# Optimization experiments

Measured on AMD Instinct MI355X. Metric: run time of the kernel, lower is better.

## Reference

```python
import jax, jax.numpy as jnp
import numpy as np

N_NODES = 50000
N_EDGES = 800000
IN_DIM = 100

def setup_inputs() -> dict:
    key = jax.random.key(0)
    ks = jax.random.split(key, 12)
    nf = jax.random.normal(ks[0], (3, IN_DIM), dtype=jnp.float32)
    tid = jax.random.randint(ks[1], (N_NODES,), 0, 4)
    xr = jax.random.normal(ks[2], (N_NODES, IN_DIM), dtype=jnp.float32)
    # nodes of type 0/1/2 get exact prototype rows; type 3 ('edge') gets random rows
    x = jnp.where((tid < 3)[:, None], nf[jnp.clip(tid, 0, 2)], xr)
    edge_index = jax.random.randint(ks[3], (2, N_EDGES), 0, N_NODES, dtype=jnp.int32)
    def w(k, fi, fo):
        return jax.random.normal(k, (fi, fo), dtype=jnp.float32) * (1.0 / np.sqrt(fi))
    return {
        'x': x, 'node_feature': nf, 'edge_index': edge_index,
        'W1': w(ks[4], 100, 512), 'b1': jnp.zeros((512,), jnp.float32),
        'W2': w(ks[5], 512, 256), 'b2': jnp.zeros((256,), jnp.float32),
        'W3': w(ks[6], 256, 128), 'b3': jnp.zeros((128,), jnp.float32),
        'W4': w(ks[7], 128, 200), 'b4': jnp.zeros((200,), jnp.float32),
    }

def _gcn_forward(x, edge_index, W1, b1, W2, b2, W3, b3, W4, b4):
    N = x.shape[0]
    loop = jnp.arange(N, dtype=edge_index.dtype)
    src = jnp.concatenate([edge_index[0], loop])
    dst = jnp.concatenate([edge_index[1], loop])
    deg = jax.ops.segment_sum(jnp.ones_like(src, dtype=x.dtype), dst, num_segments=N)
    dinv = jnp.where(deg > 0, jax.lax.rsqrt(deg), 0.0)
    norm = dinv[src] * dinv[dst]  # symmetric GCN normalization with self-loops
    def gcn(h, W, b):
        h = h @ W
        agg = jax.ops.segment_sum(h[src] * norm[:, None], dst, num_segments=N)
        return agg + b
    out = jax.nn.relu(gcn(x, W1, b1))
    out = jax.nn.relu(gcn(out, W2, b2))
    out = jax.nn.relu(gcn(out, W3, b3))
    out = jax.nn.relu(gcn(out, W4, b4))
    return out

def _cat_mean(x, out, node_feature):
    # Vectorized replacement of the per-node python loop: output slot order is
    # init(nf0)->0, accept(nf2)->1, edge(other)->2, common(nf1)->3, matching the
    # original append order when all groups are nonempty.
    eq = jnp.all(x[:, None, :] == node_feature[None, :, :], axis=-1)  # [N,3]
    group = jnp.where(eq[:, 0], 0, jnp.where(eq[:, 1], 3, jnp.where(eq[:, 2], 1, 2)))
    sums = jax.ops.segment_sum(out, group, num_segments=4)            # [4,D]
    cnt = jax.ops.segment_sum(jnp.ones((x.shape[0],), out.dtype), group, num_segments=4)
    means = jnp.where(cnt[:, None] > 0, sums / jnp.maximum(cnt, 1.0)[:, None], 0.0)
    return means.reshape(1, -1)  # [1, 4*D]

def reference(x, node_feature, edge_index, W1, b1, W2, b2, W3, b3, W4, b4):
    out = _gcn_forward(x, edge_index, W1, b1, W2, b2, W3, b3, W4, b4)
    return _cat_mean(x, out, node_feature)
```

## Files before the change

kernel.cpp:

```cpp
#include <hip/hip_runtime.h>
#include <stdint.h>

typedef __attribute__((ext_vector_type(8))) short bf16x8;
typedef __attribute__((ext_vector_type(4))) float f32x4;

__device__ __forceinline__ float bf2f(ushort h) {
    union { uint u; float f; } v; v.u = ((uint)h) << 16; return v.f;
}
__device__ __forceinline__ ushort f2bf(float f) {
    union { float f; uint u; } v; v.f = f;
    uint u = v.u;
    return (ushort)((u + 0x7fffu + ((u >> 16) & 1u)) >> 16);
}

__device__ __forceinline__ void gll(const ushort* g, ushort* l) {
    __builtin_amdgcn_global_load_lds(
        (const __attribute__((address_space(1))) void*)g,
        (__attribute__((address_space(3))) void*)l, 16, 0, 0);
}


__global__ void k_prep(const uint* __restrict__ xu, const uint* __restrict__ nfu,
                       ushort* __restrict__ xb, int* __restrict__ gid,
                       unsigned char* __restrict__ gidb, int NN) {
    int wid = blockIdx.x * 4 + (threadIdx.x >> 6);
    int lane = threadIdx.x & 63;
    if (wid >= NN) return;
    int c0 = lane * 2;
    uint w = 0u;
    int m0 = 1, m1 = 1, m2 = 1;
    if (c0 < 100) {
        uint2 xv = *(const uint2*)&xu[(size_t)wid * 100 + c0];
        uint2 a = *(const uint2*)&nfu[c0];
        uint2 bb = *(const uint2*)&nfu[100 + c0];
        uint2 c = *(const uint2*)&nfu[200 + c0];
        m0 = (xv.x == a.x) & (xv.y == a.y);
        m1 = (xv.x == bb.x) & (xv.y == bb.y);
        m2 = (xv.x == c.x) & (xv.y == c.y);
        w = (uint)f2bf(__uint_as_float(xv.x)) | ((uint)f2bf(__uint_as_float(xv.y)) << 16);
    }
    int e0 = __all(m0), e1 = __all(m1), e2 = __all(m2);
    *(uint*)&xb[(size_t)wid * 128 + c0] = w;
    if (lane == 0) {
        gid[wid] = e0 ? 0 : (e1 ? 3 : (e2 ? 1 : 2));
        gidb[wid] = (unsigned char)(e0 ? 0 : (e1 ? 1 : (e2 ? 2 : 3)));
    }
}


__global__ void k_deg(const int* __restrict__ src, const int* __restrict__ dst, int E,
                      const unsigned char* __restrict__ gidb,
                      int* __restrict__ cnt3, int* __restrict__ cntP,
                      int* __restrict__ slot) {
    int e = blockIdx.x * 256 + threadIdx.x;
    if (e >= E) return;
    int d = dst[e];
    int t = gidb[src[e]];
    int s;
    if (t == 3) s = atomicAdd(&cnt3[d], 1);
    else        s = atomicAdd(&cntP[d], 1);
    slot[e] = s | (t << 28);
}


__device__ __forceinline__ void tr2_one(const float* __restrict__ W,
                                        ushort* __restrict__ WTh, ushort* __restrict__ WTl,
                                        int K, int Nc, int KP, int idx) {
    int n = idx / KP, k = idx % KP;
    float w = (n < Nc && k < K) ? W[(size_t)k * Nc + n] : 0.0f;
    ushort hi = f2bf(w);
    ushort lo = f2bf(w - bf2f(hi));
    WTh[idx] = hi;
    WTl[idx] = lo;
}

__global__ void k_wsplit(const float* __restrict__ W1, const float* __restrict__ W2,
                         const float* __restrict__ W3, const float* __restrict__ W4,
                         ushort* __restrict__ WT1h, ushort* __restrict__ WT1l,
                         ushort* __restrict__ WT2h, ushort* __restrict__ WT2l,
                         ushort* __restrict__ WT3h, ushort* __restrict__ WT3l,
                         ushort* __restrict__ WT4h, ushort* __restrict__ WT4l) {
    int idx = blockIdx.x * 256 + threadIdx.x;
    if (idx < 65536) tr2_one(W1, WT1h, WT1l, 100, 512, 128, idx);
    else if (idx < 196608) tr2_one(W2, WT2h, WT2l, 512, 256, 512, idx - 65536);
    else if (idx < 229376) tr2_one(W3, WT3h, WT3l, 256, 128, 256, idx - 196608);
    else if (idx < 262144) tr2_one(W4, WT4h, WT4l, 128, 200, 128, idx - 229376);
}


__global__ void k_scanA(const int* __restrict__ cnt3, const int* __restrict__ cntP,
                        int* __restrict__ degT, int* __restrict__ offs,
                        int* __restrict__ bsum, float* __restrict__ dinv,
                        const int* __restrict__ gid, int* __restrict__ gcnt, int NN) {
    __shared__ int lds[256];
    __shared__ int cnt4[4];
    int t = threadIdx.x;
    if (t < 4) cnt4[t] = 0;
    int i = blockIdx.x * 256 + t;
    int v = (i < NN) ? (cnt3[i] + cntP[i]) : 0;
    if (i < NN) {
        degT[i] = v;
        dinv[i] = 1.0f / sqrtf((float)(v + 1));
    }
    lds[t] = v;
    __syncthreads();
    if (i < NN) atomicAdd(&cnt4[gid[i]], 1);
    for (int d = 1; d < 256; d <<= 1) {
        int u = (t >= d) ? lds[t - d] : 0;
        __syncthreads();
        lds[t] += u;
        __syncthreads();
    }
    if (i < NN) offs[i] = lds[t] - v;
    if (t == 255) bsum[blockIdx.x] = lds[255];
    __syncthreads();
    if (t < 4 && cnt4[t]) atomicAdd(&gcnt[t], cnt4[t]);
}


__global__ void k_fill(const int* __restrict__ src, const int* __restrict__ dst,
                       const int* __restrict__ slot, const int* __restrict__ cnt3, int E,
                       const float* __restrict__ dinv, const int* __restrict__ offs,
                       const int* __restrict__ bsum,
                       uint2* __restrict__ epk, int NN, int NB,
                       int* __restrict__ goffs) {
    __shared__ int sex[256];
    int t = threadIdx.x;
    int v = (t < NB) ? bsum[t] : 0;
    sex[t] = v;
    __syncthreads();
    for (int d = 1; d < 256; d <<= 1) {
        int u = (t >= d) ? sex[t - d] : 0;
        __syncthreads();
        sex[t] += u;
        __syncthreads();
    }
    int incl = sex[t];
    __syncthreads();
    sex[t] = incl - v;
    __syncthreads();
    int i = blockIdx.x * 256 + t;
    if (i < NN) goffs[i] = offs[i] + sex[i >> 8];
    if (i >= E) return;
    int s = src[i], d = dst[i];
    int sl = slot[i];
    int ty = sl >> 28;
    int sp = sl & 0x0FFFFFFF;
    int base = offs[d] + sex[d >> 8];
    int p = base + ((ty == 3) ? sp : (cnt3[d] + sp));
    epk[p] = make_uint2((uint)s | ((uint)ty << 30), __float_as_uint(dinv[s] * dinv[d]));
}


__device__ __forceinline__ uint2 ldnt_u2(const uint2* p) {
    union { unsigned long long ll; uint2 v; } r;
    r.ll = __builtin_nontemporal_load((const unsigned long long*)p);
    return r.v;
}

__device__ __forceinline__ void fma2(uint u, float w, float& a0, float& a1) {
    union { uint u; float f; } lo, hi;
    lo.u = u << 16;
    hi.u = u & 0xffff0000u;
    a0 = fmaf(w, lo.f, a0);
    a1 = fmaf(w, hi.f, a1);
}

template <int UN, int LD>
__device__ __forceinline__ void agg_step(const ushort* __restrict__ Hc,
                                         const uint2* __restrict__ epk, int e,
                                         float& a0, float& a1) {
    uint2 q[UN];
#pragma unroll
    for (int i = 0; i < UN; ++i) q[i] = ldnt_u2(epk + e + i);
    uint u[UN];
#pragma unroll
    for (int i = 0; i < UN; ++i)
        u[i] = *(const uint*)(Hc + (size_t)(q[i].x & 0x3FFFFFFFu) * LD);
#pragma unroll
    for (int i = 0; i < UN; ++i) fma2(u[i], __uint_as_float(q[i].y), a0, a1);
}

template <int LD, int NSL, bool BR>
__global__ __launch_bounds__(256) void k_aggs(
        const ushort* __restrict__ H, ushort* __restrict__ outb,
        const float* __restrict__ dinv, const int* __restrict__ offs,
        const int* __restrict__ deg, const uint2* __restrict__ epk,
        const float* __restrict__ bias, int NN, int NNpad) {
    int slice = (NSL > 1) ? (int)(blockIdx.x % NSL) : 0;
    int nb = (NSL > 1) ? (int)(blockIdx.x / NSL) : (int)blockIdx.x;
    int wv = threadIdx.x >> 6;
    int wid = nb * 4 + wv;
    int lane = threadIdx.x & 63;
    if (wid >= NNpad) return;
    int c0 = slice * 128 + lane * 2;
    ushort* op = outb + (size_t)wid * LD + c0;
    if (wid >= NN) {
        __builtin_nontemporal_store(0u, (uint*)op);
        return;
    }
    const ushort* Hc = H + c0;
    float a0 = 0.0f, a1 = 0.0f;
    {
        float di = dinv[wid];
        float sw = di * di;
        uint u = *(const uint*)(Hc + (size_t)wid * LD);
        fma2(u, sw, a0, a1);
    }
    int e = offs[wid];
    int end = e + deg[wid];
    for (; e + 16 <= end; e += 16) agg_step<16, LD>(Hc, epk, e, a0, a1);
    if (e + 8 <= end) { agg_step<8, LD>(Hc, epk, e, a0, a1); e += 8; }
    if (e + 4 <= end) { agg_step<4, LD>(Hc, epk, e, a0, a1); e += 4; }
    if (e + 2 <= end) { agg_step<2, LD>(Hc, epk, e, a0, a1); e += 2; }
    if (e < end) agg_step<1, LD>(Hc, epk, e, a0, a1);
    if (BR) {
        a0 = fmaxf(a0 + bias[c0], 0.0f);
        a1 = fmaxf(a1 + bias[c0 + 1], 0.0f);
    }
    uint w = (uint)f2bf(a0) | ((uint)f2bf(a1) << 16);
    __builtin_nontemporal_store(w, (uint*)op);
}


template <int UNB>
__device__ __forceinline__ void proto_step(const uint2* __restrict__ epk, int e,
                                           float& s0, float& s1, float& s2) {
    uint2 q[UNB];
#pragma unroll
    for (int i = 0; i < UNB; ++i) q[i] = ldnt_u2(epk + e + i);
#pragma unroll
    for (int i = 0; i < UNB; ++i) {
        int t = (int)(q[i].x >> 30);
        float w = __uint_as_float(q[i].y);
        s0 += (t == 0) ? w : 0.f;
        s1 += (t == 1) ? w : 0.f;
        s2 += (t == 2) ? w : 0.f;
    }
}

__global__ __launch_bounds__(256) void k_agg1(
        const ushort* __restrict__ H, const float* __restrict__ nf,
        ushort* __restrict__ outb,
        const float* __restrict__ dinv, const int* __restrict__ offs,
        const int* __restrict__ degT, const int* __restrict__ cnt3,
        const uint2* __restrict__ epk, int NN, int NNpad) {
    int wid = (int)((blockIdx.x * blockDim.x + threadIdx.x) >> 6);
    int lane = threadIdx.x & 63;
    if (wid >= NNpad) return;
    int c0 = lane * 2;
    ushort* op = outb + (size_t)wid * 128 + c0;
    if (wid >= NN) {
        __builtin_nontemporal_store(0u, (uint*)op);
        return;
    }
    const ushort* Hc = H + c0;
    float a0 = 0.0f, a1 = 0.0f;
    {
        float di = dinv[wid];
        float sw = di * di;
        uint u = *(const uint*)(Hc + (size_t)wid * 128);
        fma2(u, sw, a0, a1);
    }
    int beg = offs[wid];
    int d3 = cnt3[wid];
    int dT = degT[wid];
    int e = beg, endA = beg + d3;
    for (; e + 8 <= endA; e += 8) agg_step<8, 128>(Hc, epk, e, a0, a1);
    if (e + 4 <= endA) { agg_step<4, 128>(Hc, epk, e, a0, a1); e += 4; }
    if (e + 2 <= endA) { agg_step<2, 128>(Hc, epk, e, a0, a1); e += 2; }
    if (e < endA) agg_step<1, 128>(Hc, epk, e, a0, a1);
    float s0 = 0.f, s1 = 0.f, s2 = 0.f;
    e = endA;
    int endB = beg + dT;
    for (; e + 8 <= endB; e += 8) proto_step<8>(epk, e, s0, s1, s2);
    if (e + 4 <= endB) { proto_step<4>(epk, e, s0, s1, s2); e += 4; }
    if (e + 2 <= endB) { proto_step<2>(epk, e, s0, s1, s2); e += 2; }
    if (e < endB) proto_step<1>(epk, e, s0, s1, s2);
    if (c0 < 100) {
        float p00 = bf2f(f2bf(nf[c0]));
        float p01 = bf2f(f2bf(nf[c0 + 1]));
        float p10 = bf2f(f2bf(nf[100 + c0]));
        float p11 = bf2f(f2bf(nf[100 + c0 + 1]));
        float p20 = bf2f(f2bf(nf[200 + c0]));
        float p21 = bf2f(f2bf(nf[200 + c0 + 1]));
        a0 += s0 * p00 + s1 * p10 + s2 * p20;
        a1 += s0 * p01 + s1 * p11 + s2 * p21;
    }
    uint w = (uint)f2bf(a0) | ((uint)f2bf(a1) << 16);
    __builtin_nontemporal_store(w, (uint*)op);
}


template <bool BR, int OUT>
__global__ __launch_bounds__(256) void k_gemm(
        const ushort* __restrict__ A,
        const ushort* __restrict__ Bh, const ushort* __restrict__ Bl,
        const float* __restrict__ bias,
        ushort* __restrict__ Cb,
        int Nc, int K, int tNb,
        const int* __restrict__ gid, float* __restrict__ gsum, int NN) {
    __shared__ union {
        ushort st[3][128 * 32];
        float epi[64 * 132];
    } sm;
    __shared__ int gcode[64];
    int bm = blockIdx.x / tNb, bn = blockIdx.x % tNb;
    int m0 = bm * 128, n0 = bn * 128;
    int wv = threadIdx.x >> 6, lane = threadIdx.x & 63;
    int l15 = lane & 15, quad = lane >> 4;
    const ushort* gsrc;
    ushort* ldst;
    int ng;
    if (wv == 0)      { gsrc = A  + (size_t)m0 * K;        ldst = sm.st[0];        ng = 4; }
    else if (wv == 1) { gsrc = A  + (size_t)(m0 + 64) * K; ldst = sm.st[0] + 2048; ng = 4; }
    else if (wv == 2) { gsrc = Bh + (size_t)n0 * K;        ldst = sm.st[1];        ng = 8; }
    else              { gsrc = Bl + (size_t)n0 * K;        ldst = sm.st[2];        ng = 8; }
    const ushort* gBase = gsrc + (size_t)(lane >> 2) * K + (lane & 3) * 8;
    int wm = (wv >> 1) * 64, wn = (wv & 1) * 64;
    const ushort* sA_ = sm.st[0];
    const ushort* sBh_ = sm.st[1];
    const ushort* sBl_ = sm.st[2];
    f32x4 acc[4][4] = {};
    for (int k0 = 0; k0 < K; k0 += 32) {
        for (int i = 0; i < ng; ++i)
            gll(gBase + (size_t)(16 * i) * K + k0, ldst + i * 512);
        __syncthreads();
        bf16x8 Af[4], Bfh[4], Bfl[4];
#pragma unroll
        for (int i = 0; i < 4; ++i) {
            int ra = (wm + 16 * i + l15) * 32 + quad * 8;
            int rb = (wn + 16 * i + l15) * 32 + quad * 8;
            Af[i]  = *(const bf16x8*)(sA_ + ra);
            Bfh[i] = *(const bf16x8*)(sBh_ + rb);
            Bfl[i] = *(const bf16x8*)(sBl_ + rb);
        }
#pragma unroll
        for (int mi = 0; mi < 4; ++mi)
#pragma unroll
            for (int ni = 0; ni < 4; ++ni) {
                acc[mi][ni] = __builtin_amdgcn_mfma_f32_16x16x32_bf16(Af[mi], Bfh[ni], acc[mi][ni], 0, 0, 0);
                acc[mi][ni] = __builtin_amdgcn_mfma_f32_16x16x32_bf16(Af[mi], Bfl[ni], acc[mi][ni], 0, 0, 0);
            }
        __syncthreads();
    }
    float bia[4] = {0.f, 0.f, 0.f, 0.f};
    if (BR) {
#pragma unroll
        for (int ni = 0; ni < 4; ++ni) {
            int col = n0 + wn + 16 * ni + l15;
            if (col < Nc) bia[ni] = bias[col];
        }
    }
    float* epi = sm.epi;
    int t = threadIdx.x;
    float s0 = 0.f, s1 = 0.f, s2 = 0.f, s3 = 0.f;
    int colR = t & 127, rg = t >> 7;
    for (int half = 0; half < 2; ++half) {
        if ((wv >> 1) == half) {
#pragma unroll
            for (int mi = 0; mi < 4; ++mi)
#pragma unroll
                for (int r = 0; r < 4; ++r) {
                    int rl = mi * 16 + quad * 4 + r;
#pragma unroll
                    for (int ni = 0; ni < 4; ++ni) {
                        float v = acc[mi][ni][r];
                        if (BR) v = fmaxf(v + bia[ni], 0.0f);
                        epi[rl * 132 + wn + ni * 16 + l15] = v;
                    }
                }
        }
        if (OUT == 2 && t < 64) {
            int grow = m0 + half * 64 + t;
            gcode[t] = (grow < NN) ? gid[grow] : -1;
        }
        __syncthreads();
        if (OUT == 2) {
#pragma unroll 4
            for (int r = 0; r < 32; ++r) {
                int row = rg * 32 + r;
                int g = gcode[row];
                float v = epi[row * 132 + colR];
                s0 += (g == 0) ? v : 0.f;
                s1 += (g == 1) ? v : 0.f;
                s2 += (g == 2) ? v : 0.f;
                s3 += (g == 3) ? v : 0.f;
            }
        } else {
#pragma unroll
            for (int j = 0; j < 16; ++j) {
                int e = (j * 256 + t) * 2;
                int rl = e >> 7, cl = e & 127;
                int grow = m0 + half * 64 + rl;
                int gcol = n0 + cl;
                float v0 = epi[rl * 132 + cl];
                float v1 = epi[rl * 132 + cl + 1];
                *(uint*)&Cb[(size_t)grow * Nc + gcol] = (uint)f2bf(v0) | ((uint)f2bf(v1) << 16);
            }
        }
        __syncthreads();
    }
    if (OUT == 2) {
        if (rg == 1) {
            epi[colR * 4 + 0] = s0; epi[colR * 4 + 1] = s1;
            epi[colR * 4 + 2] = s2; epi[colR * 4 + 3] = s3;
        }
        __syncthreads();
        if (rg == 0) {
            s0 += epi[colR * 4 + 0]; s1 += epi[colR * 4 + 1];
            s2 += epi[colR * 4 + 2]; s3 += epi[colR * 4 + 3];
            int gcol = n0 + colR;
            if (gcol < Nc) {
                atomicAdd(&gsum[0 * Nc + gcol], s0);
                atomicAdd(&gsum[1 * Nc + gcol], s1);
                atomicAdd(&gsum[2 * Nc + gcol], s2);
                atomicAdd(&gsum[3 * Nc + gcol], s3);
            }
        }
    }
}


__global__ void k_final(const float* __restrict__ gsum, const int* __restrict__ gcnt,
                        float* __restrict__ out) {
    int j = blockIdx.x * blockDim.x + threadIdx.x;
    if (j >= 800) return;
    int c = gcnt[j / 200];
    out[j] = (c > 0) ? gsum[j] / (float)c : 0.0f;
}


extern "C" void kernel_launch(void* const* d_in, const int* in_sizes, int n_in,
                              void* d_out, int out_size, void* d_ws, size_t ws_size,
                              hipStream_t stream) {
    const float* x  = (const float*)d_in[0];
    const float* nf = (const float*)d_in[1];
    const int* ei   = (const int*)d_in[2];
    const float* W1 = (const float*)d_in[3];
    const float* b1 = (const float*)d_in[4];
    const float* W2 = (const float*)d_in[5];
    const float* b2 = (const float*)d_in[6];
    const float* W3 = (const float*)d_in[7];
    const float* b3 = (const float*)d_in[8];
    const float* W4 = (const float*)d_in[9];
    const float* b4 = (const float*)d_in[10];
    float* out = (float*)d_out;

    const int NN = in_sizes[0] / 100;
    const int E  = in_sizes[2] / 2;
    const int MPAD = ((NN + 127) / 128) * 128;
    const int NB = (NN + 255) / 256;
    const int PB = (NN + 3) / 4;
    const int EB = (E + 255) / 256;
    const int TB = 1024;
    const int* src = ei;
    const int* dst = ei + E;

    char* p = (char*)d_ws;
    auto alloc = [&](size_t bytes) -> char* {
        char* r = p;
        p += (bytes + 255) & ~(size_t)255;
        return r;
    };
    char* zz = p;
    int*   cnt3 = (int*)alloc((size_t)NN * 4);
    int*   cntP = (int*)alloc((size_t)NN * 4);
    float* gsum = (float*)alloc(800 * 4);
    int*   gcnt = (int*)alloc(256);
    size_t zz_bytes = (size_t)(p - zz);
    int*   degT = (int*)alloc((size_t)NN * 4);
    int*   slot = (int*)alloc((size_t)E * 4);
    float* dinv = (float*)alloc((size_t)NN * 4);
    int*   offs = (int*)alloc((size_t)NN * 4);
    int*   goffs = (int*)alloc((size_t)NN * 4);
    int*   bsum = (int*)alloc(1024);
    int*   gid  = (int*)alloc((size_t)NN * 4);
    unsigned char* gidb = (unsigned char*)alloc((size_t)NN);
    uint2* epk  = (uint2*)alloc((size_t)E * 8);
    ushort* WT1h = (ushort*)alloc((size_t)512 * 128 * 2);
    ushort* WT1l = (ushort*)alloc((size_t)512 * 128 * 2);
    ushort* WT2h = (ushort*)alloc((size_t)256 * 512 * 2);
    ushort* WT2l = (ushort*)alloc((size_t)256 * 512 * 2);
    ushort* WT3h = (ushort*)alloc((size_t)128 * 256 * 2);
    ushort* WT3l = (ushort*)alloc((size_t)128 * 256 * 2);
    ushort* WT4h = (ushort*)alloc((size_t)256 * 128 * 2);
    ushort* WT4l = (ushort*)alloc((size_t)256 * 128 * 2);
    ushort* xb = (ushort*)alloc((size_t)NN * 128 * 2);
    ushort* P1 = (ushort*)alloc((size_t)MPAD * 128 * 2);
    ushort* H1 = (ushort*)alloc((size_t)MPAD * 512 * 2);
    ushort* T2 = (ushort*)alloc((size_t)MPAD * 256 * 2);
    ushort* H2 = (ushort*)alloc((size_t)MPAD * 256 * 2);
    ushort* T3 = (ushort*)alloc((size_t)MPAD * 128 * 2);
    ushort* H3 = (ushort*)alloc((size_t)MPAD * 128 * 2);
    ushort* P4 = (ushort*)alloc((size_t)MPAD * 128 * 2);

    hipMemsetAsync(zz, 0, zz_bytes, stream);

    k_prep<<<PB, 256, 0, stream>>>((const uint*)x, (const uint*)nf, xb, gid, gidb, NN);
    k_deg<<<EB, 256, 0, stream>>>(src, dst, E, gidb, cnt3, cntP, slot);
    k_wsplit<<<TB, 256, 0, stream>>>(W1, W2, W3, W4,
        WT1h, WT1l, WT2h, WT2l, WT3h, WT3l, WT4h, WT4l);
    k_scanA<<<NB, 256, 0, stream>>>(cnt3, cntP, degT, offs, bsum, dinv, gid, gcnt, NN);
    k_fill<<<EB, 256, 0, stream>>>(src, dst, slot, cnt3, E, dinv, offs, bsum, epk, NN, NB, goffs);

    int aggBlocks = MPAD / 4;
    int mB = MPAD / 128;

    k_agg1<<<aggBlocks, 256, 0, stream>>>(xb, nf, P1, dinv, goffs, degT, cnt3, epk, NN, MPAD);
    k_gemm<true, 1><<<mB * 4, 256, 0, stream>>>(P1, WT1h, WT1l, b1, H1, 512, 128, 4, nullptr, nullptr, 0);
    k_gemm<false, 1><<<mB * 2, 256, 0, stream>>>(H1, WT2h, WT2l, nullptr, T2, 256, 512, 2, nullptr, nullptr, 0);
    k_aggs<256, 2, true><<<aggBlocks * 2, 256, 0, stream>>>(T2, H2, dinv, goffs, degT, epk, b2, NN, MPAD);
    k_gemm<false, 1><<<mB * 1, 256, 0, stream>>>(H2, WT3h, WT3l, nullptr, T3, 128, 256, 1, nullptr, nullptr, 0);
    k_aggs<128, 1, true><<<aggBlocks, 256, 0, stream>>>(T3, H3, dinv, goffs, degT, epk, b3, NN, MPAD);
    k_aggs<128, 1, false><<<aggBlocks, 256, 0, stream>>>(H3, P4, dinv, goffs, degT, epk, nullptr, NN, MPAD);
    k_gemm<true, 2><<<mB * 2, 256, 0, stream>>>(P4, WT4h, WT4l, b4, nullptr, 200, 128, 2, gid, gsum, NN);

    k_final<<<4, 256, 0, stream>>>(gsum, gcnt, out);
}
```

Measured before the change: 435.6 us.

## Double-buffer GEMM LDS tiles to overlap global loads with MFMA

Turns the GEMM's single-stage LDS staging into two alternating buffers. The next K-slice is prefetched with global_load_lds while the MFMAs run on the current slice, and vmcnt waits plus raw s_barrier replace the full __syncthreads. This is meant to hide global load latency behind compute, at the cost of doubling LDS staging from 24KB to 48KB, which may lower occupancy. The hand-written waitcnt counts and the dropped memory fences add correctness risk, since the LDS reads may not be properly ordered against the async writes.

New measurement: 422.6 us. 1.03x faster.

```diff
diff --git a/kernel.cpp b/kernel.cpp
--- a/kernel.cpp
+++ b/kernel.cpp
@@ -301,7 +301,7 @@
         int Nc, int K, int tNb,
         const int* __restrict__ gid, float* __restrict__ gsum, int NN) {
     __shared__ union {
-        ushort st[3][128 * 32];
+        ushort st[2][3][128 * 32];
         float epi[64 * 132];
     } sm;
     __shared__ int gcode[64];
@@ -310,22 +310,36 @@
     int wv = threadIdx.x >> 6, lane = threadIdx.x & 63;
     int l15 = lane & 15, quad = lane >> 4;
     const ushort* gsrc;
-    ushort* ldst;
-    int ng;
-    if (wv == 0)      { gsrc = A  + (size_t)m0 * K;        ldst = sm.st[0];        ng = 4; }
-    else if (wv == 1) { gsrc = A  + (size_t)(m0 + 64) * K; ldst = sm.st[0] + 2048; ng = 4; }
-    else if (wv == 2) { gsrc = Bh + (size_t)n0 * K;        ldst = sm.st[1];        ng = 8; }
-    else              { gsrc = Bl + (size_t)n0 * K;        ldst = sm.st[2];        ng = 8; }
+    int plane, woff, ng;
+    if (wv == 0)      { gsrc = A  + (size_t)m0 * K;        plane = 0; woff = 0;    ng = 4; }
+    else if (wv == 1) { gsrc = A  + (size_t)(m0 + 64) * K; plane = 0; woff = 2048; ng = 4; }
+    else if (wv == 2) { gsrc = Bh + (size_t)n0 * K;        plane = 1; woff = 0;    ng = 8; }
+    else              { gsrc = Bl + (size_t)n0 * K;        plane = 2; woff = 0;    ng = 8; }
     const ushort* gBase = gsrc + (size_t)(lane >> 2) * K + (lane & 3) * 8;
+    ushort* lBase = &sm.st[0][0][0] + plane * 4096 + woff;
+    const ushort* sAll = &sm.st[0][0][0];
     int wm = (wv >> 1) * 64, wn = (wv & 1) * 64;
-    const ushort* sA_ = sm.st[0];
-    const ushort* sBh_ = sm.st[1];
-    const ushort* sBl_ = sm.st[2];
     f32x4 acc[4][4] = {};
-    for (int k0 = 0; k0 < K; k0 += 32) {
-        for (int i = 0; i < ng; ++i)
-            gll(gBase + (size_t)(16 * i) * K + k0, ldst + i * 512);
-        __syncthreads();
+    int nk = K >> 5;
+    for (int i = 0; i < ng; ++i)
+        gll(gBase + (size_t)(16 * i) * K, lBase + i * 512);
+    for (int k = 0; k < nk; ++k) {
+        int cur = k & 1;
+        if (k + 1 < nk) {
+            ushort* l2 = lBase + (cur ^ 1) * 12288;
+            const ushort* g2 = gBase + (k + 1) * 32;
+            for (int i = 0; i < ng; ++i)
+                gll(g2 + (size_t)(16 * i) * K, l2 + i * 512);
+            if (ng == 4) asm volatile("s_waitcnt vmcnt(4)" ::: "memory");
+            else         asm volatile("s_waitcnt vmcnt(8)" ::: "memory");
+        } else {
+            asm volatile("s_waitcnt vmcnt(0)" ::: "memory");
+        }
+        __builtin_amdgcn_s_barrier();
+        __builtin_amdgcn_sched_barrier(0);
+        const ushort* sA_  = sAll + cur * 12288;
+        const ushort* sBh_ = sA_ + 4096;
+        const ushort* sBl_ = sA_ + 8192;
         bf16x8 Af[4], Bfh[4], Bfl[4];
 #pragma unroll
         for (int i = 0; i < 4; ++i) {
@@ -342,8 +356,9 @@
                 acc[mi][ni] = __builtin_amdgcn_mfma_f32_16x16x32_bf16(Af[mi], Bfh[ni], acc[mi][ni], 0, 0, 0);
                 acc[mi][ni] = __builtin_amdgcn_mfma_f32_16x16x32_bf16(Af[mi], Bfl[ni], acc[mi][ni], 0, 0, 0);
             }
-        __syncthreads();
-    }
+        __builtin_amdgcn_s_barrier();
+    }
+    __builtin_amdgcn_sched_barrier(0);
     float bia[4] = {0.f, 0.f, 0.f, 0.f};
     if (BR) {
 #pragma unroll
```
